# Kernel optimization log

Measured on AMD Instinct MI355X. Metric: run time of the kernel, lower is better.

The kernel has to match this reference:

```python
import jax, jax.numpy as jnp
import numpy as np

B, H, W = 8, 128, 128
ITERS = 1000


def _face_conductivities(k):
    # arithmetic-mean face conductivities with edge replication at the boundary
    kp = jnp.pad(k, ((0, 0), (1, 1), (1, 1)), mode='edge')
    c = kp[:, 1:-1, 1:-1]
    kN = 0.5 * (c + kp[:, :-2, 1:-1])
    kS = 0.5 * (c + kp[:, 2:, 1:-1])
    kW = 0.5 * (c + kp[:, 1:-1, :-2])
    kE = 0.5 * (c + kp[:, 1:-1, 2:])
    return kN, kS, kW, kE


def gauss_solver(conductivity, iterations):
    """Jacobi-style relaxation of steady diffusion div(k grad T)=0.
    Dirichlet BC: T=1 at top row, T=0 at bottom row; zero-flux (edge
    replication) on the left/right sides. Vectorized over batch."""
    kN, kS, kW, kE = _face_conductivities(conductivity)
    denom = kN + kS + kW + kE  # precomputed outside the iteration loop
    T0 = jnp.zeros_like(conductivity).at[:, 0, :].set(1.0)

    def step(T, _):
        Tp = jnp.pad(T, ((0, 0), (1, 1), (1, 1)), mode='edge')
        Tn = (kN * Tp[:, :-2, 1:-1] + kS * Tp[:, 2:, 1:-1]
              + kW * Tp[:, 1:-1, :-2] + kE * Tp[:, 1:-1, 2:]) / denom
        # re-impose Dirichlet boundary rows
        Tn = Tn.at[:, 0, :].set(1.0).at[:, -1, :].set(0.0)
        return Tn, None

    T, _ = jax.lax.scan(step, T0, None, length=iterations)
    return T


def flux_kappa(conductivity, Ts):
    # Jy = -k * dT/dy, padded back to full grid; kappa = total flux across mid row
    Jy = -conductivity[:, :-1, :] * (Ts[:, 1:, :] - Ts[:, :-1, :]) / 1.0
    Jy = jnp.pad(Jy, ((0, 0), (0, 1), (0, 0)), mode='constant', constant_values=0)
    kappas = jnp.sum(Jy[:, conductivity.shape[1] // 2, :], axis=-1)
    return kappas


def setup_inputs() -> dict:
    key = jax.random.key(0)
    # strictly positive conductivity field in [0.1, 1.0)
    u = jax.random.uniform(key, (B, H, W), dtype=jnp.float32)
    conductivity = 0.1 + 0.9 * u
    return {"conductivity": conductivity, "iterations": ITERS}


def reference(conductivity, iterations):
    T = gauss_solver(conductivity, iterations)
    return flux_kappa(conductivity, T)
```

## Files before the change

### kernel.cpp

```cpp
#include <hip/hip_runtime.h>


#define GH 128
#define GW 128
#define NW 16
#define RPW 8
#define NT 1024

typedef float v2f __attribute__((ext_vector_type(2)));

__device__ __forceinline__ float dpp_shr1(float old_v, float src) {
    return __int_as_float(__builtin_amdgcn_update_dpp(
        __float_as_int(old_v), __float_as_int(src), 0x138, 0xf, 0xf, false));
}
__device__ __forceinline__ float dpp_shl1(float old_v, float src) {
    return __int_as_float(__builtin_amdgcn_update_dpp(
        __float_as_int(old_v), __float_as_int(src), 0x130, 0xf, 0xf, false));
}

__device__ __forceinline__ v2f pk_mul_yx(v2f a, v2f b) {
    v2f d;
    asm("v_pk_mul_f32 %0, %1, %2 op_sel:[0,1] op_sel_hi:[1,0]"
        : "=v"(d) : "v"(a), "v"(b));
    return d;
}
__device__ __forceinline__ v2f pk_fma(v2f a, v2f b, v2f c) {
    v2f d;
    asm("v_pk_fma_f32 %0, %1, %2, %3 op_sel:[0,0,0] op_sel_hi:[1,1,1]"
        : "=v"(d) : "v"(a), "v"(b), "v"(c));
    return d;
}

__global__ void __launch_bounds__(NT)
__attribute__((amdgpu_waves_per_eu(4, 4)))
jacobi_flux_kernel(const float* __restrict__ k_all,
                   const int* __restrict__ iters_p,
                   float* __restrict__ out)
{
    __shared__ __align__(16) v2f sTop[2][NW][64];
    __shared__ __align__(16) v2f sBot[2][NW][64];

    const int b   = blockIdx.x;
    const int tid = threadIdx.x;
    const int l   = tid & 63;
    const int w   = tid >> 6;
    const int R0  = w * RPW;
    const int c0  = l * 2;
    const float* kb = k_all + b * GH * GW;
    const int iters = *iters_p;

    const int wUp = (w == 0)      ? 0      : w - 1;
    const int wDn = (w == NW - 1) ? NW - 1 : w + 1;
    const bool gTop = (w == 0);
    const bool gBot = (w == NW - 1);

    v2f rN[RPW], rS[RPW], cM[RPW], cLR[RPW];
    #pragma unroll
    for (int i = 0; i < RPW; ++i) {
        const int r  = R0 + i;
        const int ru = (r == 0)      ? 0      : r - 1;
        const int rd = (r == GH - 1) ? GH - 1 : r + 1;
        float v[2][4];
        #pragma unroll
        for (int jj = 0; jj < 2; ++jj) {
            const int c  = c0 + jj;
            const int cl = (c == 0)      ? 0      : c - 1;
            const int cr = (c == GW - 1) ? GW - 1 : c + 1;
            float kc = kb[r * GW + c];
            float kn = 0.5f * (kc + kb[ru * GW + c]);
            float ks = 0.5f * (kc + kb[rd * GW + c]);
            float kw = 0.5f * (kc + kb[r * GW + cl]);
            float ke = 0.5f * (kc + kb[r * GW + cr]);
            float inv = 1.0f / (kn + ks + kw + ke);
            v[jj][0] = kn * inv; v[jj][1] = ks * inv;
            v[jj][2] = kw * inv; v[jj][3] = ke * inv;
        }
        rN[i]  = (v2f){v[0][0], v[1][0]};
        rS[i]  = (v2f){v[0][1], v[1][1]};
        cM[i]  = (v2f){v[0][3], v[1][2]};
        cLR[i] = (v2f){v[0][2], v[1][3]};
    }

    v2f A[RPW], B[RPW];
    #pragma unroll
    for (int i = 0; i < RPW; ++i)
        A[i] = (R0 + i == 0) ? (v2f){1.0f, 1.0f} : (v2f){0.0f, 0.0f};

    sTop[0][w][l] = A[0];
    sBot[0][w][l] = A[RPW - 1];
    __syncthreads();

    auto step = [&](const v2f (&src)[RPW], v2f (&dst)[RPW], int rp, int wp) {
        v2f hu = sBot[rp][wUp][l];
        v2f hd = sTop[rp][wDn][l];

        #pragma unroll
        for (int i = 0; i < RPW; ++i) {
            v2f cc = src[i];
            v2f s;
            s.x = dpp_shr1(cc.x, cc.y);
            s.y = dpp_shl1(cc.y, cc.x);
            v2f up = (i == 0)       ? hu : src[i - 1];
            v2f dn = (i == RPW - 1) ? hd : src[i + 1];
            dst[i] = pk_fma(rN[i], up,
                     pk_fma(rS[i], dn,
                     pk_fma(cLR[i], s, pk_mul_yx(cM[i], cc))));
        }
        if (gTop) dst[0]       = (v2f){1.0f, 1.0f};
        if (gBot) dst[RPW - 1] = (v2f){0.0f, 0.0f};

        sTop[wp][w][l] = dst[0];
        sBot[wp][w][l] = dst[RPW - 1];
        __syncthreads();
    };

    const int nPairs = iters >> 1;
    for (int it = 0; it < nPairs; ++it) {
        step(A, B, 0, 1);
        step(B, A, 1, 0);
    }
    if (iters & 1) {
        step(A, B, 0, 1);
        #pragma unroll
        for (int i = 0; i < RPW; ++i) A[i] = B[i];
    }

    if (w == 8) {
        float partial = kb[64 * GW + c0]     * (A[1].x - A[0].x)
                      + kb[64 * GW + c0 + 1] * (A[1].y - A[0].y);
        #pragma unroll
        for (int off = 32; off > 0; off >>= 1)
            partial += __shfl_down(partial, off, 64);
        if (l == 0) out[b] = -partial;
    }
}

extern "C" void kernel_launch(void* const* d_in, const int* in_sizes, int n_in,
                              void* d_out, int out_size, void* d_ws, size_t ws_size,
                              hipStream_t stream)
{
    const float* k     = (const float*)d_in[0];
    const int*   iters = (const int*)d_in[1];
    float*       out   = (float*)d_out;
    jacobi_flux_kernel<<<dim3(8), dim3(NT), 0, stream>>>(k, iters, out);
}
```

Measured before the change: 589.4 us.

## Split each batch grid across two workgroups with global-memory halo exchange

Each batch's 128x128 grid is now split between two workgroups, 16 blocks in total, so each wave handles 4 rows instead of 8. The boundary rows between the two halves are exchanged every iteration through a double-buffered workspace, using release/acquire flag spinning at agent scope. A small kernel zeroes the flags before launch. This doubles the CUs used and halves the per-iteration arithmetic per wave, but adds a global-memory round trip and a spin-wait to every one of the 1000 iterations. It also assumes both workgroups of a batch are resident at the same time.

New measurement: 1.417 ms. 140% more time.

```diff
diff --git a/kernel.cpp b/kernel.cpp
--- a/kernel.cpp
+++ b/kernel.cpp
@@ -4,7 +4,7 @@
 #define GH 128
 #define GW 128
 #define NW 16
-#define RPW 8
+#define RPW 4
 #define NT 1024
 
 typedef float v2f __attribute__((ext_vector_type(2)));
@@ -31,28 +31,41 @@
     return d;
 }
 
+__global__ void zero_flags_kernel(int* __restrict__ flags) {
+    if (threadIdx.x < 16) flags[threadIdx.x] = 0;
+}
+
 __global__ void __launch_bounds__(NT)
-__attribute__((amdgpu_waves_per_eu(4, 4)))
 jacobi_flux_kernel(const float* __restrict__ k_all,
                    const int* __restrict__ iters_p,
-                   float* __restrict__ out)
+                   float* __restrict__ out,
+                   float* __restrict__ ws)
 {
     __shared__ __align__(16) v2f sTop[2][NW][64];
     __shared__ __align__(16) v2f sBot[2][NW][64];
 
-    const int b   = blockIdx.x;
-    const int tid = threadIdx.x;
-    const int l   = tid & 63;
-    const int w   = tid >> 6;
-    const int R0  = w * RPW;
-    const int c0  = l * 2;
+    const int blk  = blockIdx.x;
+    const int half = blk >> 3;
+    const int b    = blk & 7;
+    const int tid  = threadIdx.x;
+    const int l    = tid & 63;
+    const int w    = tid >> 6;
+    const int R0   = half * 64 + w * RPW;
+    const int c0   = l * 2;
     const float* kb = k_all + b * GH * GW;
     const int iters = *iters_p;
 
+    float* haloD = ws + b * 256;
+    float* haloU = ws + 2048 + b * 256;
+    int*   fD    = (int*)ws + 4096 + b;
+    int*   fU    = (int*)ws + 4104 + b;
+
     const int wUp = (w == 0)      ? 0      : w - 1;
     const int wDn = (w == NW - 1) ? NW - 1 : w + 1;
-    const bool gTop = (w == 0);
-    const bool gBot = (w == NW - 1);
+    const bool gTop  = (half == 0 && w == 0);
+    const bool gBot  = (half == 1 && w == NW - 1);
+    const bool consU = (half == 0 && w == NW - 1);
+    const bool consD = (half == 1 && w == 0);
 
     v2f rN[RPW], rS[RPW], cM[RPW], cLR[RPW];
     #pragma unroll
@@ -88,11 +101,34 @@
 
     sTop[0][w][l] = A[0];
     sBot[0][w][l] = A[RPW - 1];
+    if (consU) {
+        ((v2f*)haloD)[l] = A[RPW - 1];
+        if (l == 0)
+            __hip_atomic_store(fD, 1, __ATOMIC_RELEASE, __HIP_MEMORY_SCOPE_AGENT);
+    }
+    if (consD) {
+        ((v2f*)haloU)[l] = A[0];
+        if (l == 0)
+            __hip_atomic_store(fU, 1, __ATOMIC_RELEASE, __HIP_MEMORY_SCOPE_AGENT);
+    }
     __syncthreads();
 
-    auto step = [&](const v2f (&src)[RPW], v2f (&dst)[RPW], int rp, int wp) {
-        v2f hu = sBot[rp][wUp][l];
-        v2f hd = sTop[rp][wDn][l];
+    auto step = [&](const v2f (&src)[RPW], v2f (&dst)[RPW], int rp, int wp, int t) {
+        v2f hu, hd;
+        if (consD) {
+            while (__hip_atomic_load(fD, __ATOMIC_ACQUIRE,
+                                     __HIP_MEMORY_SCOPE_AGENT) < t + 1) {}
+            hu = ((const v2f*)(haloD + (t & 1) * 128))[l];
+        } else {
+            hu = sBot[rp][wUp][l];
+        }
+        if (consU) {
+            while (__hip_atomic_load(fU, __ATOMIC_ACQUIRE,
+                                     __HIP_MEMORY_SCOPE_AGENT) < t + 1) {}
+            hd = ((const v2f*)(haloU + (t & 1) * 128))[l];
+        } else {
+            hd = sTop[rp][wDn][l];
+        }
 
         #pragma unroll
         for (int i = 0; i < RPW; ++i) {
@@ -111,21 +147,35 @@
 
         sTop[wp][w][l] = dst[0];
         sBot[wp][w][l] = dst[RPW - 1];
+
+        if (consU) {
+            ((v2f*)(haloD + ((t + 1) & 1) * 128))[l] = dst[RPW - 1];
+            if (l == 0)
+                __hip_atomic_store(fD, t + 2, __ATOMIC_RELEASE,
+                                   __HIP_MEMORY_SCOPE_AGENT);
+        }
+        if (consD) {
+            ((v2f*)(haloU + ((t + 1) & 1) * 128))[l] = dst[0];
+            if (l == 0)
+                __hip_atomic_store(fU, t + 2, __ATOMIC_RELEASE,
+                                   __HIP_MEMORY_SCOPE_AGENT);
+        }
         __syncthreads();
     };
 
+    int t = 0;
     const int nPairs = iters >> 1;
     for (int it = 0; it < nPairs; ++it) {
-        step(A, B, 0, 1);
-        step(B, A, 1, 0);
+        step(A, B, 0, 1, t); ++t;
+        step(B, A, 1, 0, t); ++t;
     }
     if (iters & 1) {
-        step(A, B, 0, 1);
+        step(A, B, 0, 1, t); ++t;
         #pragma unroll
         for (int i = 0; i < RPW; ++i) A[i] = B[i];
     }
 
-    if (w == 8) {
+    if (half == 1 && w == 0) {
         float partial = kb[64 * GW + c0]     * (A[1].x - A[0].x)
                       + kb[64 * GW + c0 + 1] * (A[1].y - A[0].y);
         #pragma unroll
@@ -142,5 +192,7 @@
     const float* k     = (const float*)d_in[0];
     const int*   iters = (const int*)d_in[1];
     float*       out   = (float*)d_out;
-    jacobi_flux_kernel<<<dim3(8), dim3(NT), 0, stream>>>(k, iters, out);
+    int*         flags = (int*)d_ws + 4096;
+    zero_flags_kernel<<<dim3(1), dim3(64), 0, stream>>>(flags);
+    jacobi_flux_kernel<<<dim3(16), dim3(NT), 0, stream>>>(k, iters, out, (float*)d_ws);
 }
```

## Split each batch grid across two blocks with overlapping halos and flag exchange

Applied to the files above, without the earlier changes.

Each batch's 128-row grid is now split across two workgroups instead of one. Each workgroup owns 80 rows (rows 48–79 overlap) at 5 rows per wave instead of 8, and the update is done in place. Every 16 Jacobi steps the two halves swap 16 overlap rows through global workspace memory, synchronised by release/acquire flags that a small prelaunch kernel zeroes. This roughly halves per-step work per wave and spreads the work over twice as many CUs. In exchange it adds redundant compute in the overlap, periodic global-memory round trips with spin-waits, and a dependence on all 16 blocks being resident at once.

Result: slower. 825.1 us (+40.0%).

```diff
diff --git a/kernel.cpp b/kernel.cpp
--- a/kernel.cpp
+++ b/kernel.cpp
@@ -4,8 +4,9 @@
 #define GH 128
 #define GW 128
 #define NW 16
-#define RPW 8
+#define RPW 5
 #define NT 1024
+#define GSTEP 16
 
 typedef float v2f __attribute__((ext_vector_type(2)));
 
@@ -31,28 +32,41 @@
     return d;
 }
 
+__global__ void zero_flags_kernel(int* __restrict__ flags) {
+    if (threadIdx.x < 16) flags[threadIdx.x] = 0;
+}
+
 __global__ void __launch_bounds__(NT)
-__attribute__((amdgpu_waves_per_eu(4, 4)))
 jacobi_flux_kernel(const float* __restrict__ k_all,
                    const int* __restrict__ iters_p,
-                   float* __restrict__ out)
+                   float* __restrict__ out,
+                   float* __restrict__ ws)
 {
     __shared__ __align__(16) v2f sTop[2][NW][64];
     __shared__ __align__(16) v2f sBot[2][NW][64];
 
-    const int b   = blockIdx.x;
-    const int tid = threadIdx.x;
-    const int l   = tid & 63;
-    const int w   = tid >> 6;
-    const int R0  = w * RPW;
-    const int c0  = l * 2;
+    const int blk  = blockIdx.x;
+    const int half = blk >> 3;
+    const int b    = blk & 7;
+    const int tid  = threadIdx.x;
+    const int l    = tid & 63;
+    const int w    = tid >> 6;
+    const int base = half * 48;
+    const int R0   = base + w * RPW;
+    const int c0   = l * 2;
     const float* kb = k_all + b * GH * GW;
     const int iters = *iters_p;
 
+    float* bufU = ws + b * 4096;
+    float* bufL = ws + 32768 + b * 4096;
+    int* flags  = (int*)(ws + 65536);
+    int* myFlag      = (half == 0) ? (flags + b)     : (flags + 8 + b);
+    int* partnerFlag = (half == 0) ? (flags + 8 + b) : (flags + b);
+
     const int wUp = (w == 0)      ? 0      : w - 1;
     const int wDn = (w == NW - 1) ? NW - 1 : w + 1;
-    const bool gTop = (w == 0);
-    const bool gBot = (w == NW - 1);
+    const bool gTop = (half == 0 && w == 0);
+    const bool gBot = (half == 1 && w == NW - 1);
 
     v2f rN[RPW], rS[RPW], cM[RPW], cLR[RPW];
     #pragma unroll
@@ -81,7 +95,7 @@
         cLR[i] = (v2f){v[0][2], v[1][3]};
     }
 
-    v2f A[RPW], B[RPW];
+    v2f A[RPW];
     #pragma unroll
     for (int i = 0; i < RPW; ++i)
         A[i] = (R0 + i == 0) ? (v2f){1.0f, 1.0f} : (v2f){0.0f, 0.0f};
@@ -90,44 +104,84 @@
     sBot[0][w][l] = A[RPW - 1];
     __syncthreads();
 
-    auto step = [&](const v2f (&src)[RPW], v2f (&dst)[RPW], int rp, int wp) {
+    auto F = [&](int i, v2f up, v2f cc, v2f dn) -> v2f {
+        v2f s;
+        s.x = dpp_shr1(cc.x, cc.y);
+        s.y = dpp_shl1(cc.y, cc.x);
+        return pk_fma(rN[i], up,
+               pk_fma(rS[i], dn,
+               pk_fma(cLR[i], s, pk_mul_yx(cM[i], cc))));
+    };
+
+    auto stepf = [&](int rp, int wp) {
         v2f hu = sBot[rp][wUp][l];
         v2f hd = sTop[rp][wDn][l];
-
-        #pragma unroll
-        for (int i = 0; i < RPW; ++i) {
-            v2f cc = src[i];
-            v2f s;
-            s.x = dpp_shr1(cc.x, cc.y);
-            s.y = dpp_shl1(cc.y, cc.x);
-            v2f up = (i == 0)       ? hu : src[i - 1];
-            v2f dn = (i == RPW - 1) ? hd : src[i + 1];
-            dst[i] = pk_fma(rN[i], up,
-                     pk_fma(rS[i], dn,
-                     pk_fma(cLR[i], s, pk_mul_yx(cM[i], cc))));
-        }
-        if (gTop) dst[0]       = (v2f){1.0f, 1.0f};
-        if (gBot) dst[RPW - 1] = (v2f){0.0f, 0.0f};
-
-        sTop[wp][w][l] = dst[0];
-        sBot[wp][w][l] = dst[RPW - 1];
+        v2f o1 = A[1], o2 = A[2], o3 = A[3];
+        A[1] = F(1, A[0], o1, o2);
+        A[2] = F(2, o1, o2, o3);
+        A[3] = F(3, o2, o3, A[4]);
+        A[0] = F(0, hu, A[0], o1);
+        A[4] = F(4, o3, A[4], hd);
+        if (gTop) A[0] = (v2f){1.0f, 1.0f};
+        if (gBot) A[4] = (v2f){0.0f, 0.0f};
+        sTop[wp][w][l] = A[0];
+        sBot[wp][w][l] = A[4];
         __syncthreads();
     };
 
-    const int nPairs = iters >> 1;
-    for (int it = 0; it < nPairs; ++it) {
-        step(A, B, 0, 1);
-        step(B, A, 1, 0);
+    auto exchange = [&](int e) {
+        const int p = e & 1;
+        #pragma unroll
+        for (int i = 0; i < RPW; ++i) {
+            const int r = R0 + i;
+            if (half == 0) {
+                if (r >= 48 && r <= 63)
+                    ((v2f*)(bufU + p * 2048 + (r - 48) * 128))[l] = A[i];
+            } else {
+                if (r >= 64 && r <= 79)
+                    ((v2f*)(bufL + p * 2048 + (r - 64) * 128))[l] = A[i];
+            }
+        }
+        __threadfence();
+        __syncthreads();
+        if (tid == 0)
+            __hip_atomic_store(myFlag, e, __ATOMIC_RELEASE,
+                               __HIP_MEMORY_SCOPE_AGENT);
+        const bool reader = (half == 0) ? (R0 + RPW - 1 >= 64) : (R0 <= 63);
+        if (reader) {
+            while (__hip_atomic_load(partnerFlag, __ATOMIC_ACQUIRE,
+                                     __HIP_MEMORY_SCOPE_AGENT) < e) {}
+            #pragma unroll
+            for (int i = 0; i < RPW; ++i) {
+                const int r = R0 + i;
+                if (half == 0) {
+                    if (r >= 64)
+                        A[i] = ((const v2f*)(bufL + p * 2048 + (r - 64) * 128))[l];
+                } else {
+                    if (r <= 63)
+                        A[i] = ((const v2f*)(bufU + p * 2048 + (r - 48) * 128))[l];
+                }
+            }
+            sTop[0][w][l] = A[0];
+            sBot[0][w][l] = A[RPW - 1];
+        }
+        __syncthreads();
+    };
+
+    int t = 0;
+    while (t + GSTEP <= iters) {
+        #pragma unroll
+        for (int s = 0; s < GSTEP / 2; ++s) { stepf(0, 1); stepf(1, 0); }
+        t += GSTEP;
+        if (t < iters) exchange(t >> 4);
     }
-    if (iters & 1) {
-        step(A, B, 0, 1);
-        #pragma unroll
-        for (int i = 0; i < RPW; ++i) A[i] = B[i];
-    }
-
-    if (w == 8) {
-        float partial = kb[64 * GW + c0]     * (A[1].x - A[0].x)
-                      + kb[64 * GW + c0 + 1] * (A[1].y - A[0].y);
+    const int rem = iters - t;
+    for (int s = 0; s + 2 <= rem; s += 2) { stepf(0, 1); stepf(1, 0); }
+    if (rem & 1) stepf(0, 1);
+
+    if (half == 1 && w == 3) {
+        float partial = kb[64 * GW + c0]     * (A[2].x - A[1].x)
+                      + kb[64 * GW + c0 + 1] * (A[2].y - A[1].y);
         #pragma unroll
         for (int off = 32; off > 0; off >>= 1)
             partial += __shfl_down(partial, off, 64);
@@ -142,5 +196,7 @@
     const float* k     = (const float*)d_in[0];
     const int*   iters = (const int*)d_in[1];
     float*       out   = (float*)d_out;
-    jacobi_flux_kernel<<<dim3(8), dim3(NT), 0, stream>>>(k, iters, out);
-}
+    int*         flags = (int*)d_ws + 65536;
+    zero_flags_kernel<<<dim3(1), dim3(64), 0, stream>>>(flags);
+    jacobi_flux_kernel<<<dim3(16), dim3(NT), 0, stream>>>(k, iters, out, (float*)d_ws);
+}
```
